# Performance work log

Measured on AMD Instinct MI355X. Metric: run time of the kernel, lower is better.

The kernel has to match this reference:

```python
import jax, jax.numpy as jnp
import numpy as np

DIM = 1024
STEPS = 4
LEAK = 0.9
RESET = 0.0
EPS = 1e-6


def setup_inputs() -> dict:
    key = jax.random.key(0)
    ks = jax.random.split(key, 5)
    sc = 1.0 / np.sqrt(DIM)
    return {
        "x": jax.random.normal(ks[0], (4, 4096, DIM), dtype=jnp.float32),
        "W_in": jax.random.normal(ks[1], (DIM, DIM), dtype=jnp.float32) * sc,
        "W_inh": jax.random.normal(ks[2], (DIM, DIM), dtype=jnp.float32) * sc,
        "W_out": jax.random.normal(ks[3], (DIM, DIM), dtype=jnp.float32) * sc,
        "threshold_vec": jnp.full((DIM,), 0.5, dtype=jnp.float32),
        "norm_weight": jnp.ones((DIM,), dtype=jnp.float32),
    }


def _rmsnorm(y, w):
    # RMSNorm: y * rsqrt(mean(y^2)) * w
    ms = jnp.mean(y * y, axis=-1, keepdims=True)
    return y * jax.lax.rsqrt(ms + EPS) * w


def reference(x, W_in, W_inh, W_out, threshold_vec, norm_weight):
    # x: [B, L, D]
    membrane = jnp.zeros_like(x)
    current = x @ W_in.T  # same every step; computed once (identical math)
    spike_sum = jnp.zeros_like(x)
    prev_spike = None
    for step in range(STEPS):
        membrane = membrane + current
        if step > 0:
            membrane = membrane - 0.1 * (prev_spike @ W_inh.T)
        fire_mask = (membrane > threshold_vec).astype(x.dtype)
        fire_soft = jax.nn.sigmoid((membrane - threshold_vec) * 10.0)
        # straight-through estimator: hard mask fwd, sigmoid grad
        fire_mask_grad = fire_mask - jax.lax.stop_gradient(fire_soft) + fire_soft
        spike = fire_mask_grad * membrane
        spike_sum = spike_sum + spike
        prev_spike = spike
        membrane = (membrane * (1.0 - fire_mask) + RESET * fire_mask) * LEAK
    spike_total = spike_sum / float(STEPS)
    lif_out = spike_total @ W_out.T
    fired_any = (jnp.abs(spike_total) > 1e-6).astype(x.dtype)
    y = x * (1.0 - 0.5 * fired_any) + 0.5 * lif_out
    x_lif = _rmsnorm(y, norm_weight)
    return x_lif, spike_total, membrane
```

## Files before the change

kernel.cpp:

```cpp
#include <hip/hip_runtime.h>
#include <cmath>

#define N_ROWS 16384
#define DIM 1024
#define MARGIN 5e-5
#define MAX_EVENTS 4194304
#define BATCH 8


__global__ __launch_bounds__(64) void zero_cnt(int* cnt) {
  if (threadIdx.x == 0 && blockIdx.x == 0) cnt[0] = 0;
}

__device__ inline void record_event(int* cnt, int* ev, int r, int s, int c) {
  int idx = atomicAdd(cnt, 1);
  if (idx < MAX_EVENTS) ev[idx] = (r << 12) | (s << 10) | c;
}

template<typename TA, int STEP, bool WRITE_SPK>
__global__ __launch_bounds__(256) void gemm_lif(
    const TA* __restrict__ A, const float* __restrict__ B,
    double* __restrict__ cur, double* __restrict__ mem,
    double* __restrict__ spk_out, float* __restrict__ ssum,
    const float* __restrict__ thr, int* cnt, int* ev)
{
  __shared__ double As[16][130];
  __shared__ double Bs[16][66];
  const int tid  = threadIdx.x;
  const int tx   = tid & 15;
  const int ty   = tid >> 4;
  const int col0 = blockIdx.x * 64;
  const int row0 = blockIdx.y * 128;

  const int ar  = tid >> 1;
  const int akc = (tid & 1) * 8;
  const int bc  = tid >> 2;
  const int bkc = (tid & 3) * 4;

  double acc[8][4] = {};

  for (int k0 = 0; k0 < DIM; k0 += 16) {
    const TA* ap = &A[(size_t)(row0 + ar) * DIM + (size_t)(k0 + akc)];
#pragma unroll
    for (int u = 0; u < 8; ++u) As[akc + u][ar] = (double)ap[u];
    const float* bp = &B[(size_t)(col0 + bc) * DIM + (size_t)(k0 + bkc)];
#pragma unroll
    for (int u = 0; u < 4; ++u) Bs[bkc + u][bc] = (double)bp[u];
    __syncthreads();
#pragma unroll
    for (int kk = 0; kk < 16; ++kk) {
      double a[8], b[4];
#pragma unroll
      for (int i = 0; i < 8; ++i) a[i] = As[kk][ty * 8 + i];
#pragma unroll
      for (int j = 0; j < 4; ++j) b[j] = Bs[kk][tx * 4 + j];
#pragma unroll
      for (int i = 0; i < 8; ++i)
#pragma unroll
        for (int j = 0; j < 4; ++j)
          acc[i][j] = fma(a[i], b[j], acc[i][j]);
    }
    __syncthreads();
  }

#pragma unroll
  for (int i = 0; i < 8; ++i)
#pragma unroll
    for (int j = 0; j < 4; ++j) {
      const int r = row0 + ty * 8 + i;
      const int c = col0 + tx * 4 + j;
      const size_t e = (size_t)r * DIM + c;
      double m;
      if (STEP == 0) {
        m = acc[i][j];
        cur[e] = m;
      } else {
        const double m1 = __dadd_rn(mem[e], cur[e]);
        const double t2 = __dmul_rn(0.1, acc[i][j]);
        m = __dsub_rn(m1, t2);
      }
      const double t = (double)thr[c];
      if (fabs(m - t) < MARGIN) record_event(cnt, ev, r, STEP, c);
      const bool fire = m > t;
      const double s = fire ? m : 0.0;
      if (WRITE_SPK) spk_out[e] = s;
      if (STEP == 0) ssum[e] = (float)s;
      else           ssum[e] += (float)s;
      mem[e] = fire ? 0.0 : __dmul_rn(m, 0.9);
    }
}

__global__ __launch_bounds__(256) void init_mid(
    const double* __restrict__ mem, const float* __restrict__ ssum,
    float* __restrict__ memlo, float* __restrict__ memhi,
    float* __restrict__ out1)
{
  size_t base = (size_t)blockIdx.x * 2048 + threadIdx.x;
#pragma unroll
  for (int v = 0; v < 8; ++v) {
    size_t e = base + (size_t)v * 256;
    float f = (float)mem[e];
    memlo[e] = f;
    memhi[e] = f;
    out1[e]  = __fmul_rn(ssum[e], 0.25f);
  }
}

__device__ inline void atomicMinF(float* p, float v) {
  unsigned* u = (unsigned*)p;
  unsigned old = __float_as_uint(*p);
  while (__uint_as_float(old) > v) {
    unsigned assumed = old;
    old = atomicCAS(u, assumed, __float_as_uint(v));
    if (old == assumed) break;
  }
}
__device__ inline void atomicMaxF(float* p, float v) {
  unsigned* u = (unsigned*)p;
  unsigned old = __float_as_uint(*p);
  while (__uint_as_float(old) < v) {
    unsigned assumed = old;
    old = atomicCAS(u, assumed, __float_as_uint(v));
    if (old == assumed) break;
  }
}

__global__ __launch_bounds__(256) void transpose_w(
    const float* __restrict__ W, float* __restrict__ Wt)
{
  __shared__ float t[32][33];
  const int bx = blockIdx.x & 31, by = blockIdx.x >> 5;
  const int x = threadIdx.x & 31, y0 = (threadIdx.x >> 5) << 2;
#pragma unroll
  for (int u = 0; u < 4; ++u)
    t[y0 + u][x] = W[(size_t)(by * 32 + y0 + u) * DIM + bx * 32 + x];
  __syncthreads();
#pragma unroll
  for (int u = 0; u < 4; ++u)
    Wt[(size_t)(bx * 32 + y0 + u) * DIM + by * 32 + x] = t[x][y0 + u];
}

__global__ __launch_bounds__(256) void phase2d(
    const double* __restrict__ cur, const float* __restrict__ Wt,
    const float* __restrict__ thr, const int* __restrict__ cnt,
    const int* __restrict__ ev, float* __restrict__ memlo,
    float* __restrict__ memhi)
{
  __shared__ float spk_l[BATCH][DIM];
  int total = cnt[0];
  if (total > MAX_EVENTS) total = MAX_EVENTS;
  const int tid = threadIdx.x;

  double tv[4];
#pragma unroll
  for (int q = 0; q < 4; ++q) tv[q] = (double)thr[tid + q * 256];

  for (int base = blockIdx.x * BATCH; base < total;
       base += gridDim.x * BATCH) {
    const int nb = min(BATCH, total - base);
    int rr[BATCH], sfv[BATCH], efv[BATCH];
#pragma unroll
    for (int v = 0; v < BATCH; ++v) {
      const int code = ev[base + min(v, nb - 1)];
      rr[v]  = code >> 12;
      sfv[v] = (code >> 10) & 3;
      efv[v] = code & 1023;
    }

    double memr[BATCH][4];

    __syncthreads();
#pragma unroll
    for (int v = 0; v < BATCH; ++v) {
      const double* cr = cur + (size_t)rr[v] * DIM;
#pragma unroll
      for (int q = 0; q < 4; ++q) {
        const int j = tid + q * 256;
        const double m = cr[j];
        bool fire = m > tv[q];
        if (sfv[v] == 0 && j == efv[v]) fire = !fire;
        spk_l[v][j] = (float)(fire ? m : 0.0);
        memr[v][q]  = fire ? 0.0 : __dmul_rn(m, 0.9);
      }
    }
    __syncthreads();

    for (int s = 1; s < 4; ++s) {
      double acc[BATCH][4] = {};
#pragma unroll 2
      for (int e = 0; e < DIM; ++e) {
        const float* w = Wt + (size_t)e * DIM + tid;
        double wd[4];
#pragma unroll
        for (int q = 0; q < 4; ++q) wd[q] = (double)w[q * 256];
#pragma unroll
        for (int v = 0; v < BATCH; ++v) {
          const double sp = (double)spk_l[v][e];
#pragma unroll
          for (int q = 0; q < 4; ++q)
            acc[v][q] = fma(sp, wd[q], acc[v][q]);
        }
      }
      __syncthreads();
#pragma unroll
      for (int v = 0; v < BATCH; ++v) {
        const double* cr = cur + (size_t)rr[v] * DIM;
#pragma unroll
        for (int q = 0; q < 4; ++q) {
          const int j = tid + q * 256;
          const double m1 = __dadd_rn(memr[v][q], cr[j]);
          const double t2 = __dmul_rn(0.1, acc[v][q]);
          const double m  = __dsub_rn(m1, t2);
          bool fire = m > tv[q];
          if (sfv[v] == s && j == efv[v]) fire = !fire;
          spk_l[v][j] = (float)(fire ? m : 0.0);
          memr[v][q]  = fire ? 0.0 : __dmul_rn(m, 0.9);
        }
      }
      __syncthreads();
    }

    for (int v = 0; v < nb; ++v) {
#pragma unroll
      for (int q = 0; q < 4; ++q) {
        const int j = tid + q * 256;
        const float f = (float)memr[v][q];
        const size_t g = (size_t)rr[v] * DIM + j;
        atomicMinF(&memlo[g], f);
        atomicMaxF(&memhi[g], f);
      }
    }
  }
}

__global__ __launch_bounds__(256) void finalize2(
    const float* __restrict__ memlo, const float* __restrict__ memhi,
    float* __restrict__ out2)
{
  size_t base = (size_t)blockIdx.x * 2048 + threadIdx.x;
#pragma unroll
  for (int v = 0; v < 8; ++v) {
    size_t e = base + (size_t)v * 256;
    out2[e] = __fmul_rn(__fadd_rn(memlo[e], memhi[e]), 0.5f);
  }
}

__global__ __launch_bounds__(256) void gemm_wout_epi(
    const float* __restrict__ Asp, const float* __restrict__ B,
    const float* __restrict__ x, float* __restrict__ y, int K)
{
  __shared__ float As[64][17];
  __shared__ float Bs[64][17];
  const int tid  = threadIdx.x;
  const int tx   = tid & 15;
  const int ty   = tid >> 4;
  const int col0 = blockIdx.x * 64;
  const int row0 = blockIdx.y * 64;
  const int lr   = tid >> 2;
  const int lc   = (tid & 3) << 2;

  float acc[4][4] = {};

  for (int k0 = 0; k0 < K; k0 += 16) {
#pragma unroll
    for (int u = 0; u < 4; ++u) {
      As[lr][lc + u] = Asp[(size_t)(row0 + lr) * K + (size_t)(k0 + lc + u)];
      Bs[lr][lc + u] = B[(size_t)(col0 + lr) * K + (size_t)(k0 + lc + u)];
    }
    __syncthreads();
#pragma unroll
    for (int kk = 0; kk < 16; ++kk) {
      float a[4], b[4];
#pragma unroll
      for (int i = 0; i < 4; ++i) a[i] = As[ty * 4 + i][kk];
#pragma unroll
      for (int j = 0; j < 4; ++j) b[j] = Bs[tx * 4 + j][kk];
#pragma unroll
      for (int i = 0; i < 4; ++i)
#pragma unroll
        for (int j = 0; j < 4; ++j)
          acc[i][j] = fmaf(a[i], b[j], acc[i][j]);
    }
    __syncthreads();
  }

#pragma unroll
  for (int i = 0; i < 4; ++i)
#pragma unroll
    for (int j = 0; j < 4; ++j) {
      size_t idx = (size_t)(row0 + ty * 4 + i) * DIM + (size_t)(col0 + tx * 4 + j);
      float st    = Asp[idx] * 0.25f;
      float fired = (fabsf(st) > 1e-6f) ? 1.0f : 0.0f;
      float lif   = 0.25f * acc[i][j];
      y[idx] = x[idx] * (1.0f - 0.5f * fired) + 0.5f * lif;
    }
}

__global__ __launch_bounds__(256) void rmsnorm_k(
    const float* __restrict__ y, const float* __restrict__ wn,
    float* __restrict__ out)
{
  const int row = blockIdx.x;
  const int tid = threadIdx.x;
  const float4 v = reinterpret_cast<const float4*>(y + (size_t)row * DIM)[tid];
  double ss = (double)v.x * v.x + (double)v.y * v.y +
              (double)v.z * v.z + (double)v.w * v.w;
#pragma unroll
  for (int off = 32; off; off >>= 1) ss += __shfl_down(ss, off, 64);
  __shared__ double warr[4];
  if ((tid & 63) == 0) warr[tid >> 6] = ss;
  __syncthreads();
  double tot = warr[0] + warr[1] + warr[2] + warr[3];
  float r = rsqrtf((float)(tot * (1.0 / 1024.0)) + 1e-6f);
  const float4 wv = reinterpret_cast<const float4*>(wn)[tid];
  float4 o;
  o.x = v.x * r * wv.x;
  o.y = v.y * r * wv.y;
  o.z = v.z * r * wv.z;
  o.w = v.w * r * wv.w;
  reinterpret_cast<float4*>(out + (size_t)row * DIM)[tid] = o;
}

extern "C" void kernel_launch(void* const* d_in, const int* in_sizes, int n_in,
                              void* d_out, int out_size, void* d_ws, size_t ws_size,
                              hipStream_t stream) {
  const float* x     = (const float*)d_in[0];
  const float* W_in  = (const float*)d_in[1];
  const float* W_inh = (const float*)d_in[2];
  const float* W_out = (const float*)d_in[3];
  const float* thr   = (const float*)d_in[4];
  const float* nw    = (const float*)d_in[5];

  const size_t nd = (size_t)N_ROWS * DIM;
  float* out0 = (float*)d_out;
  float* out1 = out0 + nd;
  float* out2 = out1 + nd;

  char* p = (char*)d_ws;
  double* cur  = (double*)p; p += nd * sizeof(double);
  double* mem  = (double*)p; p += nd * sizeof(double);
  double* spk0 = (double*)p; p += nd * sizeof(double);
  double* spk1 = (double*)p; p += nd * sizeof(double);
  float*  ssum = (float*)p;  p += nd * sizeof(float);

  float* memlo = (float*)spk0;
  float* memhi = (float*)spk0 + nd;
  float* ybuf  = (float*)spk1;
  float* Wt    = out0;
  int* evcnt = (int*)out2;
  int* ev    = (int*)out2 + 4;

  dim3 ggrid2(DIM / 64, N_ROWS / 128);
  dim3 ggrid(DIM / 64, N_ROWS / 64);
  const int egrid = (int)(nd / 2048);

  zero_cnt<<<1, 64, 0, stream>>>(evcnt);
  transpose_w<<<1024, 256, 0, stream>>>(W_inh, Wt);
  gemm_lif<float, 0, true><<<ggrid2, 256, 0, stream>>>(
      x, W_in, cur, mem, spk0, ssum, thr, evcnt, ev);
  gemm_lif<double, 1, true><<<ggrid2, 256, 0, stream>>>(
      spk0, W_inh, cur, mem, spk1, ssum, thr, evcnt, ev);
  gemm_lif<double, 2, true><<<ggrid2, 256, 0, stream>>>(
      spk1, W_inh, cur, mem, spk0, ssum, thr, evcnt, ev);
  gemm_lif<double, 3, false><<<ggrid2, 256, 0, stream>>>(
      spk0, W_inh, cur, mem, spk1, ssum, thr, evcnt, ev);
  init_mid<<<egrid, 256, 0, stream>>>(mem, ssum, memlo, memhi, out1);
  phase2d<<<2048, 256, 0, stream>>>(cur, Wt, thr, evcnt, ev, memlo, memhi);
  finalize2<<<egrid, 256, 0, stream>>>(memlo, memhi, out2);
  gemm_wout_epi<<<ggrid, 256, 0, stream>>>(ssum, W_out, x, ybuf, DIM);
  rmsnorm_k<<<N_ROWS, 256, 0, stream>>>(ybuf, nw, out0);
}
```

Before: 5.003 ms.

## Vectorize LDS reads in fp64 GEMM and remap event-replay kernel to 1024 threads

In the fp64 LIF GEMM, each thread now reads its A and B fragments from shared memory as double2 vectors, and its output columns are remapped to a strided pattern (two adjacent columns, then the same pair 32 columns later) to cut LDS bank conflicts and instruction count. The event-replay kernel is restructured so each of 1024 threads owns one column. Spikes are stored interleaved in pairs so they can be read as float2 broadcasts, and per-thread register arrays shrink from 8x4 to 8. The grid drops to 512 blocks, which changes occupancy and the per-block work balance. Register pressure and the number of resident waves per CU may shift in either direction.

Result: slower. 5.176 ms (+3.5%).

```diff
diff --git a/kernel.cpp b/kernel.cpp
--- a/kernel.cpp
+++ b/kernel.cpp
@@ -49,11 +49,15 @@
     __syncthreads();
 #pragma unroll
     for (int kk = 0; kk < 16; ++kk) {
-      double a[8], b[4];
-#pragma unroll
-      for (int i = 0; i < 8; ++i) a[i] = As[kk][ty * 8 + i];
-#pragma unroll
-      for (int j = 0; j < 4; ++j) b[j] = Bs[kk][tx * 4 + j];
+      const double2 a01 = *reinterpret_cast<const double2*>(&As[kk][ty * 8]);
+      const double2 a23 = *reinterpret_cast<const double2*>(&As[kk][ty * 8 + 2]);
+      const double2 a45 = *reinterpret_cast<const double2*>(&As[kk][ty * 8 + 4]);
+      const double2 a67 = *reinterpret_cast<const double2*>(&As[kk][ty * 8 + 6]);
+      const double2 b01 = *reinterpret_cast<const double2*>(&Bs[kk][tx * 2]);
+      const double2 b23 = *reinterpret_cast<const double2*>(&Bs[kk][tx * 2 + 32]);
+      const double a[8] = {a01.x, a01.y, a23.x, a23.y,
+                           a45.x, a45.y, a67.x, a67.y};
+      const double b[4] = {b01.x, b01.y, b23.x, b23.y};
 #pragma unroll
       for (int i = 0; i < 8; ++i)
 #pragma unroll
@@ -68,7 +72,7 @@
 #pragma unroll
     for (int j = 0; j < 4; ++j) {
       const int r = row0 + ty * 8 + i;
-      const int c = col0 + tx * 4 + j;
+      const int c = col0 + tx * 2 + (j & 1) + (j >> 1) * 32;
       const size_t e = (size_t)r * DIM + c;
       double m;
       if (STEP == 0) {
@@ -140,95 +144,78 @@
     Wt[(size_t)(bx * 32 + y0 + u) * DIM + by * 32 + x] = t[x][y0 + u];
 }
 
-__global__ __launch_bounds__(256) void phase2d(
+__global__ __launch_bounds__(1024) void phase2e(
     const double* __restrict__ cur, const float* __restrict__ Wt,
     const float* __restrict__ thr, const int* __restrict__ cnt,
     const int* __restrict__ ev, float* __restrict__ memlo,
     float* __restrict__ memhi)
 {
-  __shared__ float spk_l[BATCH][DIM];
+  __shared__ float spk2[4][DIM][2];
   int total = cnt[0];
   if (total > MAX_EVENTS) total = MAX_EVENTS;
-  const int tid = threadIdx.x;
-
-  double tv[4];
-#pragma unroll
-  for (int q = 0; q < 4; ++q) tv[q] = (double)thr[tid + q * 256];
+  const int j = threadIdx.x;
+  const double tv = (double)thr[j];
 
   for (int base = blockIdx.x * BATCH; base < total;
        base += gridDim.x * BATCH) {
     const int nb = min(BATCH, total - base);
-    int rr[BATCH], sfv[BATCH], efv[BATCH];
+    int code[BATCH];
+#pragma unroll
+    for (int v = 0; v < BATCH; ++v) code[v] = ev[base + min(v, nb - 1)];
+
+    double memr[BATCH];
+
+    __syncthreads();
 #pragma unroll
     for (int v = 0; v < BATCH; ++v) {
-      const int code = ev[base + min(v, nb - 1)];
-      rr[v]  = code >> 12;
-      sfv[v] = (code >> 10) & 3;
-      efv[v] = code & 1023;
-    }
-
-    double memr[BATCH][4];
-
-    __syncthreads();
-#pragma unroll
-    for (int v = 0; v < BATCH; ++v) {
-      const double* cr = cur + (size_t)rr[v] * DIM;
-#pragma unroll
-      for (int q = 0; q < 4; ++q) {
-        const int j = tid + q * 256;
-        const double m = cr[j];
-        bool fire = m > tv[q];
-        if (sfv[v] == 0 && j == efv[v]) fire = !fire;
-        spk_l[v][j] = (float)(fire ? m : 0.0);
-        memr[v][q]  = fire ? 0.0 : __dmul_rn(m, 0.9);
-      }
+      const int r = code[v] >> 12;
+      const double m = cur[(size_t)r * DIM + j];
+      bool fire = m > tv;
+      if (((code[v] >> 10) & 3) == 0 && j == (code[v] & 1023)) fire = !fire;
+      spk2[v >> 1][j][v & 1] = (float)(fire ? m : 0.0);
+      memr[v] = fire ? 0.0 : __dmul_rn(m, 0.9);
     }
     __syncthreads();
 
     for (int s = 1; s < 4; ++s) {
-      double acc[BATCH][4] = {};
+      double acc[BATCH] = {};
 #pragma unroll 2
       for (int e = 0; e < DIM; ++e) {
-        const float* w = Wt + (size_t)e * DIM + tid;
-        double wd[4];
-#pragma unroll
-        for (int q = 0; q < 4; ++q) wd[q] = (double)w[q * 256];
-#pragma unroll
-        for (int v = 0; v < BATCH; ++v) {
-          const double sp = (double)spk_l[v][e];
-#pragma unroll
-          for (int q = 0; q < 4; ++q)
-            acc[v][q] = fma(sp, wd[q], acc[v][q]);
-        }
+        const double wd = (double)Wt[(size_t)e * DIM + j];
+        const float2 p0 = *reinterpret_cast<const float2*>(&spk2[0][e][0]);
+        const float2 p1 = *reinterpret_cast<const float2*>(&spk2[1][e][0]);
+        const float2 p2 = *reinterpret_cast<const float2*>(&spk2[2][e][0]);
+        const float2 p3 = *reinterpret_cast<const float2*>(&spk2[3][e][0]);
+        acc[0] = fma((double)p0.x, wd, acc[0]);
+        acc[1] = fma((double)p0.y, wd, acc[1]);
+        acc[2] = fma((double)p1.x, wd, acc[2]);
+        acc[3] = fma((double)p1.y, wd, acc[3]);
+        acc[4] = fma((double)p2.x, wd, acc[4]);
+        acc[5] = fma((double)p2.y, wd, acc[5]);
+        acc[6] = fma((double)p3.x, wd, acc[6]);
+        acc[7] = fma((double)p3.y, wd, acc[7]);
       }
       __syncthreads();
 #pragma unroll
       for (int v = 0; v < BATCH; ++v) {
-        const double* cr = cur + (size_t)rr[v] * DIM;
-#pragma unroll
-        for (int q = 0; q < 4; ++q) {
-          const int j = tid + q * 256;
-          const double m1 = __dadd_rn(memr[v][q], cr[j]);
-          const double t2 = __dmul_rn(0.1, acc[v][q]);
-          const double m  = __dsub_rn(m1, t2);
-          bool fire = m > tv[q];
-          if (sfv[v] == s && j == efv[v]) fire = !fire;
-          spk_l[v][j] = (float)(fire ? m : 0.0);
-          memr[v][q]  = fire ? 0.0 : __dmul_rn(m, 0.9);
-        }
+        const int r = code[v] >> 12;
+        const double m1 = __dadd_rn(memr[v], cur[(size_t)r * DIM + j]);
+        const double t2 = __dmul_rn(0.1, acc[v]);
+        const double m  = __dsub_rn(m1, t2);
+        bool fire = m > tv;
+        if (((code[v] >> 10) & 3) == s && j == (code[v] & 1023)) fire = !fire;
+        spk2[v >> 1][j][v & 1] = (float)(fire ? m : 0.0);
+        memr[v] = fire ? 0.0 : __dmul_rn(m, 0.9);
       }
       __syncthreads();
     }
 
     for (int v = 0; v < nb; ++v) {
-#pragma unroll
-      for (int q = 0; q < 4; ++q) {
-        const int j = tid + q * 256;
-        const float f = (float)memr[v][q];
-        const size_t g = (size_t)rr[v] * DIM + j;
-        atomicMinF(&memlo[g], f);
-        atomicMaxF(&memhi[g], f);
-      }
+      const int r = code[v] >> 12;
+      const float f = (float)memr[v];
+      const size_t g = (size_t)r * DIM + j;
+      atomicMinF(&memlo[g], f);
+      atomicMaxF(&memhi[g], f);
     }
   }
 }
@@ -365,7 +352,7 @@
   gemm_lif<double, 3, false><<<ggrid2, 256, 0, stream>>>(
       spk0, W_inh, cur, mem, spk1, ssum, thr, evcnt, ev);
   init_mid<<<egrid, 256, 0, stream>>>(mem, ssum, memlo, memhi, out1);
-  phase2d<<<2048, 256, 0, stream>>>(cur, Wt, thr, evcnt, ev, memlo, memhi);
+  phase2e<<<512, 1024, 0, stream>>>(cur, Wt, thr, evcnt, ev, memlo, memhi);
   finalize2<<<egrid, 256, 0, stream>>>(memlo, memhi, out2);
   gemm_wout_epi<<<ggrid, 256, 0, stream>>>(ssum, W_out, x, ybuf, DIM);
   rmsnorm_k<<<N_ROWS, 256, 0, stream>>>(ybuf, nw, out0);
```
